# Kernel optimization log

Hardware: AMD Instinct MI355X
Metric: run time of the kernel (lower is better)

## Reference

```python
import jax, jax.numpy as jnp
import numpy as np

N_NODES = 50000
N_EDGES = 1600000
IN_CH = 128
HEADS = 4
OUT_PER_HEAD = 32  # out_channels // heads with concat=True
NEG_SLOPE = 0.2    # GATConv default leaky_relu slope
SOFTMAX_EPS = 1e-16  # PyG scatter-softmax denominator eps
LN_EPS = 1e-5


def setup_inputs() -> dict:
    key = jax.random.key(0)
    ks = jax.random.split(key, 8)
    x = jax.random.normal(ks[0], (N_NODES, IN_CH), dtype=jnp.float32)
    edge_index = jax.random.randint(ks[1], (2, N_EDGES), 0, N_NODES, dtype=jnp.int32)
    W = jax.random.normal(ks[2], (IN_CH, HEADS * OUT_PER_HEAD), dtype=jnp.float32) * (1.0 / np.sqrt(IN_CH))
    att_src = jax.random.normal(ks[3], (HEADS, OUT_PER_HEAD), dtype=jnp.float32) * 0.1
    att_dst = jax.random.normal(ks[4], (HEADS, OUT_PER_HEAD), dtype=jnp.float32) * 0.1
    bias = jnp.zeros((HEADS * OUT_PER_HEAD,), dtype=jnp.float32)
    gamma = jnp.ones((HEADS * OUT_PER_HEAD,), dtype=jnp.float32)
    beta = jnp.zeros((HEADS * OUT_PER_HEAD,), dtype=jnp.float32)
    return {"x": x, "edge_index": edge_index, "W": W, "att_src": att_src,
            "att_dst": att_dst, "bias": bias, "gamma": gamma, "beta": beta}


def reference(x, edge_index, W, att_src, att_dst, bias, gamma, beta):
    N = x.shape[0]
    H, C = att_src.shape
    # GATConv default add_self_loops=True
    loop = jnp.arange(N, dtype=edge_index.dtype)
    src = jnp.concatenate([edge_index[0], loop])  # message source j
    dst = jnp.concatenate([edge_index[1], loop])  # aggregation target i

    h = (x @ W).reshape(N, H, C)                      # [N,H,C]
    a_s = jnp.einsum('nhc,hc->nh', h, att_src)        # [N,H]
    a_d = jnp.einsum('nhc,hc->nh', h, att_dst)        # [N,H]

    logits = jax.nn.leaky_relu(a_s[src] + a_d[dst], NEG_SLOPE)  # [E,H]
    # segment softmax over edges grouped by destination node
    m = jax.ops.segment_max(logits, dst, num_segments=N)        # [N,H]
    m = jnp.where(jnp.isfinite(m), m, 0.0)
    e = jnp.exp(logits - m[dst])
    s = jax.ops.segment_sum(e, dst, num_segments=N)             # [N,H]
    alpha = e / (s[dst] + SOFTMAX_EPS)                          # [E,H]

    msg = h[src] * alpha[:, :, None]                            # [E,H,C]
    out = jax.ops.segment_sum(msg, dst, num_segments=N)         # [N,H,C]
    out = out.reshape(N, H * C) + bias

    mu = out.mean(axis=-1, keepdims=True)
    var = ((out - mu) ** 2).mean(axis=-1, keepdims=True)
    y = (out - mu) / jnp.sqrt(var + LN_EPS) * gamma + beta
    return jax.nn.elu(y)
```

## Files before the change

kernel.cpp:

```cpp
#include <hip/hip_runtime.h>
#include <hip/hip_bf16.h>

typedef __hip_bfloat16 bf16;
typedef unsigned int u32;
typedef unsigned short u16;
typedef __attribute__((ext_vector_type(8))) short bf16x8;
typedef __attribute__((ext_vector_type(4))) float f32x4;

constexpr int N   = 50000;
constexpr int E   = 1600000;
constexpr int C   = 128;
constexpr int H   = 4;
constexpr int NB  = 782;
constexpr int CAP = 2560;
constexpr int CHUNK = 6250;
constexpr float NEG  = 0.2f;
constexpr float SEPS = 1e-16f;
constexpr float LEPS = 1e-5f;

__device__ __forceinline__ float lo16(u32 v) { return __uint_as_float(v << 16); }
__device__ __forceinline__ float hi16(u32 v) { return __uint_as_float(v & 0xFFFF0000u); }
__device__ __forceinline__ u16 bfbits(float f) {
    __hip_bfloat16 h = __float2bfloat16(f);
    return *reinterpret_cast<u16*>(&h);
}

__global__ __launch_bounds__(256) void k0_wprep(
    const float* __restrict__ W, u16* __restrict__ wt_hi, u16* __restrict__ wt_lo)
{
    const int i = blockIdx.x * 256 + threadIdx.x;
    const int c = i >> 7, k = i & 127;
    const float w = W[k * 128 + c];
    const __hip_bfloat16 h = __float2bfloat16(w);
    const float fh = __bfloat162float(h);
    wt_hi[i] = *(const u16*)&h;
    wt_lo[i] = bfbits(w - fh);
}

__global__ __launch_bounds__(256) void k1_mfma(
    const float* __restrict__ x,
    const u16* __restrict__ wt_hi, const u16* __restrict__ wt_lo,
    const float* __restrict__ att_s, const float* __restrict__ att_d,
    u16* __restrict__ hb, float* __restrict__ as_, float* __restrict__ ad_)
{
    constexpr int LDX = 136;
    __shared__ u16 xhi[64 * LDX];
    __shared__ u16 xlo[64 * LDX];
    const int t  = threadIdx.x;
    const int m0 = blockIdx.x * 64;

#pragma unroll
    for (int it = 0; it < 8; ++it) {
        const int idx = it * 1024 + t * 4;
        const int r = idx >> 7, c = idx & 127;
        const int gr = min(m0 + r, N - 1);
        const float4 v = *(const float4*)(x + (size_t)gr * 128 + c);
        ushort4 sh, sl;
        {
            __hip_bfloat16 h0 = __float2bfloat16(v.x);
            __hip_bfloat16 h1 = __float2bfloat16(v.y);
            __hip_bfloat16 h2 = __float2bfloat16(v.z);
            __hip_bfloat16 h3 = __float2bfloat16(v.w);
            sh.x = *(u16*)&h0; sh.y = *(u16*)&h1; sh.z = *(u16*)&h2; sh.w = *(u16*)&h3;
            sl.x = bfbits(v.x - __bfloat162float(h0));
            sl.y = bfbits(v.y - __bfloat162float(h1));
            sl.z = bfbits(v.z - __bfloat162float(h2));
            sl.w = bfbits(v.w - __bfloat162float(h3));
        }
        *(ushort4*)(xhi + r * LDX + c) = sh;
        *(ushort4*)(xlo + r * LDX + c) = sl;
    }
    __syncthreads();

    const int lane = t & 63;
    const int w    = t >> 6;
    const int arow = w * 16 + (lane & 15);
    const int akg  = lane >> 4;
    const int bcol = lane & 15;
    const int aq   = lane >> 4;

    bf16x8 Ah[4], Al[4];
#pragma unroll
    for (int ks = 0; ks < 4; ++ks) {
        Ah[ks] = *(const bf16x8*)(xhi + arow * LDX + ks * 32 + akg * 8);
        Al[ks] = *(const bf16x8*)(xlo + arow * LDX + ks * 32 + akg * 8);
    }

    f32x4 acc[8];
#pragma unroll
    for (int nt = 0; nt < 8; ++nt) acc[nt] = f32x4{0.f, 0.f, 0.f, 0.f};

#pragma unroll
    for (int nt = 0; nt < 8; ++nt) {
        const u16* bp = wt_hi + (nt * 16 + bcol) * 128 + akg * 8;
        const u16* bq = wt_lo + (nt * 16 + bcol) * 128 + akg * 8;
#pragma unroll
        for (int ks = 0; ks < 4; ++ks) {
            const bf16x8 Bh = *(const bf16x8*)(bp + ks * 32);
            const bf16x8 Bl = *(const bf16x8*)(bq + ks * 32);
            acc[nt] = __builtin_amdgcn_mfma_f32_16x16x32_bf16(Ah[ks], Bh, acc[nt], 0, 0, 0);
            acc[nt] = __builtin_amdgcn_mfma_f32_16x16x32_bf16(Al[ks], Bh, acc[nt], 0, 0, 0);
            acc[nt] = __builtin_amdgcn_mfma_f32_16x16x32_bf16(Ah[ks], Bl, acc[nt], 0, 0, 0);
        }
    }

#pragma unroll
    for (int nt = 0; nt < 8; ++nt) {
        const int ch = nt * 16 + bcol;
#pragma unroll
        for (int r = 0; r < 4; ++r) {
            const int node = m0 + w * 16 + aq * 4 + r;
            if (node < N) hb[(size_t)node * 128 + ch] = bfbits(acc[nt][r]);
        }
    }

    float ps[4][4], pd[4][4];
#pragma unroll
    for (int h = 0; h < 4; ++h) {
        const float a0 = att_s[32 * h + bcol],      a1 = att_s[32 * h + 16 + bcol];
        const float d0 = att_d[32 * h + bcol],      d1 = att_d[32 * h + 16 + bcol];
#pragma unroll
        for (int r = 0; r < 4; ++r) {
            ps[h][r] = acc[2 * h][r] * a0 + acc[2 * h + 1][r] * a1;
            pd[h][r] = acc[2 * h][r] * d0 + acc[2 * h + 1][r] * d1;
        }
    }
#pragma unroll
    for (int off = 1; off < 16; off <<= 1) {
#pragma unroll
        for (int h = 0; h < 4; ++h)
#pragma unroll
            for (int r = 0; r < 4; ++r) {
                ps[h][r] += __shfl_xor(ps[h][r], off, 64);
                pd[h][r] += __shfl_xor(pd[h][r], off, 64);
            }
    }
    if (bcol == 0) {
#pragma unroll
        for (int r = 0; r < 4; ++r) {
            const int node = m0 + w * 16 + aq * 4 + r;
            if (node < N) {
#pragma unroll
                for (int h = 0; h < 4; ++h) {
                    as_[node * H + h] = ps[h][r];
                    ad_[node * H + h] = pd[h][r];
                }
            }
        }
    }
}

__global__ __launch_bounds__(256) void kbin(
    const int* __restrict__ ei, u32* __restrict__ gcur, u32* __restrict__ pairs)
{
    __shared__ u32 lcnt[NB], lbase[NB], lfill[NB];
    const int t = threadIdx.x;
    const int base = blockIdx.x * CHUNK;
    const int nE = min(CHUNK, E - base);
    for (int i = t; i < NB; i += 256) lcnt[i] = 0;
    __syncthreads();
    for (int i = t; i < nE; i += 256)
        atomicAdd(&lcnt[((u32)ei[E + base + i]) >> 6], 1u);
    __syncthreads();
    for (int i = t; i < NB; i += 256) {
        u32 cb = lcnt[i];
        lbase[i] = cb ? atomicAdd(&gcur[i], cb) : 0u;
        lfill[i] = 0u;
    }
    __syncthreads();
    for (int i = t; i < nE; i += 256) {
        u32 src = (u32)ei[base + i];
        u32 dst = (u32)ei[E + base + i];
        u32 b = dst >> 6;
        u32 pos = atomicAdd(&lfill[b], 1u);
        pairs[(size_t)b * CAP + lbase[b] + pos] = src | ((dst & 63u) << 16);
    }
}

__global__ __launch_bounds__(64) void kscan(
    const u32* __restrict__ gcur, u32* __restrict__ bbase, int* __restrict__ row_ptr)
{
    const int t = threadIdx.x;
    u32 vals[13];
    u32 s = 0;
#pragma unroll
    for (int i = 0; i < 13; ++i) {
        int idx = t * 13 + i;
        u32 v = (idx < NB) ? gcur[idx] : 0u;
        vals[i] = s; s += v;
    }
    u32 incl = s;
#pragma unroll
    for (int off = 1; off < 64; off <<= 1) {
        u32 u = __shfl_up(incl, off, 64);
        if (t >= off) incl += u;
    }
    const u32 excl = incl - s;
#pragma unroll
    for (int i = 0; i < 13; ++i) {
        int idx = t * 13 + i;
        if (idx < NB) bbase[idx] = excl + vals[i];
    }
    if (t == 0) row_ptr[N] = E;
}

__global__ __launch_bounds__(256) void kfill2(
    const u32* __restrict__ pairs, const u32* __restrict__ gcur,
    const u32* __restrict__ bbase, int* __restrict__ row_ptr, u16* __restrict__ col)
{
    __shared__ u32 spr[CAP];
    __shared__ u16 scol[CAP];
    __shared__ int jcnt[64], joff[64], jcur[64];
    const int b = blockIdx.x, t = threadIdx.x;
    const int cntb = (int)gcur[b];
    const int base = (int)bbase[b];
    if (t < 64) jcnt[t] = 0;
    const u32* pr = pairs + (size_t)b * CAP;
    for (int i = t; i < cntb; i += 256) spr[i] = pr[i];
    __syncthreads();
    for (int i = t; i < cntb; i += 256) atomicAdd(&jcnt[spr[i] >> 16], 1);
    __syncthreads();
    if (t < 64) {
        int v = jcnt[t], incl = v;
#pragma unroll
        for (int off = 1; off < 64; off <<= 1) {
            int u = __shfl_up(incl, off, 64);
            if (t >= off) incl += u;
        }
        joff[t] = incl - v;
        const int n = b * 64 + t;
        if (n < N) row_ptr[n] = base + joff[t];
        jcur[t] = 0;
    }
    __syncthreads();
    for (int i = t; i < cntb; i += 256) {
        const u32 p = spr[i];
        const int j = p >> 16;
        const int pos = atomicAdd(&jcur[j], 1);
        scol[joff[j] + pos] = (u16)(p & 0xFFFFu);
    }
    __syncthreads();
    for (int i = t; i < cntb; i += 256) col[base + i] = scol[i];
}

__global__ __launch_bounds__(256) void kd_agg_ln(
    const int* __restrict__ row_ptr, const u16* __restrict__ col,
    const u32* __restrict__ hb, const float* __restrict__ as_,
    const float* __restrict__ ad_,
    const float* __restrict__ bias, const float* __restrict__ gamma,
    const float* __restrict__ beta, float* __restrict__ out)
{
    __shared__ float wlds[4][64];
    const int tid  = threadIdx.x;
    const int lane = tid & 63;
    const int wv   = __builtin_amdgcn_readfirstlane(tid >> 6);
    const int n    = __builtin_amdgcn_readfirstlane((int)blockIdx.x * 4 + (tid >> 6));
    if (n >= N) return;

    const int head  = lane >> 4;
    const int eoff  = lane & 15;
    const int wbase = head << 4;
    float* __restrict__ wrow = wlds[wv];

    const float adn = ad_[n * H + head];
    const float asn = as_[n * H + head];

    float ls = asn + adn;
    ls = fmaxf(ls, NEG * ls);
    const float wself = __expf(ls);
    float den = (eoff == 0) ? wself : 0.f;
    const u32 hvs = hb[n * 64 + lane];
    float num0 = wself * lo16(hvs);
    float num1 = wself * hi16(hvs);

    const int k0  = row_ptr[n];
    const int deg = row_ptr[n + 1] - k0;
    const int ntiles = (deg + 15) >> 4;

    const int cnt0 = deg < 16 ? deg : 16;
    const int cnt1 = (deg - 16) < 16 ? (deg - 16) : 16;
    int colv_cur = (eoff < cnt0) ? (int)col[k0 + eoff]      : 0;
    int colv_nxt = (eoff < cnt1) ? (int)col[k0 + 16 + eoff] : 0;
    float a_cur  = as_[colv_cur * H + head];
    int cntc = cnt0, cntn = cnt1;

    int k = k0;
    for (int t = 0; t < ntiles; ++t, k += 16) {
        const int rem2 = deg - 16 * (t + 2);
        const int cnt2 = rem2 < 16 ? rem2 : 16;
        const int cf_raw = (int)col[k + 32 + eoff];
        const int colv_f = (eoff < cnt2) ? cf_raw : 0;

        float le = a_cur + adn;
        le = fmaxf(le, NEG * le);
        const float w = (eoff < cntc) ? __expf(le) : 0.f;
        den += w;
        wrow[lane] = w;
        const int colc = colv_cur;

#define GL(i) const u32* rp##i = hb + ((size_t)(u32)__builtin_amdgcn_readlane(colc, i) << 6); \
              const u32 v##i = rp##i[lane];
        GL(0) GL(1) GL(2) GL(3) GL(4) GL(5) GL(6) GL(7)
        GL(8) GL(9) GL(10) GL(11) GL(12) GL(13) GL(14) GL(15)
#undef GL
        __builtin_amdgcn_sched_barrier(0);

        const float a_n = as_[colv_nxt * H + head];
        __builtin_amdgcn_sched_barrier(0);

        {
            const float4 wa = *(const float4*)(wrow + wbase + 0);
            num0 = fmaf(wa.x, lo16(v0), num0);  num1 = fmaf(wa.x, hi16(v0), num1);
            num0 = fmaf(wa.y, lo16(v1), num0);  num1 = fmaf(wa.y, hi16(v1), num1);
            num0 = fmaf(wa.z, lo16(v2), num0);  num1 = fmaf(wa.z, hi16(v2), num1);
            num0 = fmaf(wa.w, lo16(v3), num0);  num1 = fmaf(wa.w, hi16(v3), num1);
            const float4 wb = *(const float4*)(wrow + wbase + 4);
            num0 = fmaf(wb.x, lo16(v4), num0);  num1 = fmaf(wb.x, hi16(v4), num1);
            num0 = fmaf(wb.y, lo16(v5), num0);  num1 = fmaf(wb.y, hi16(v5), num1);
            num0 = fmaf(wb.z, lo16(v6), num0);  num1 = fmaf(wb.z, hi16(v6), num1);
            num0 = fmaf(wb.w, lo16(v7), num0);  num1 = fmaf(wb.w, hi16(v7), num1);
            const float4 wc = *(const float4*)(wrow + wbase + 8);
            num0 = fmaf(wc.x, lo16(v8), num0);  num1 = fmaf(wc.x, hi16(v8), num1);
            num0 = fmaf(wc.y, lo16(v9), num0);  num1 = fmaf(wc.y, hi16(v9), num1);
            num0 = fmaf(wc.z, lo16(v10), num0); num1 = fmaf(wc.z, hi16(v10), num1);
            num0 = fmaf(wc.w, lo16(v11), num0); num1 = fmaf(wc.w, hi16(v11), num1);
            const float4 wd = *(const float4*)(wrow + wbase + 12);
            num0 = fmaf(wd.x, lo16(v12), num0); num1 = fmaf(wd.x, hi16(v12), num1);
            num0 = fmaf(wd.y, lo16(v13), num0); num1 = fmaf(wd.y, hi16(v13), num1);
            num0 = fmaf(wd.z, lo16(v14), num0); num1 = fmaf(wd.z, hi16(v14), num1);
            num0 = fmaf(wd.w, lo16(v15), num0); num1 = fmaf(wd.w, hi16(v15), num1);
        }

        colv_cur = colv_nxt; colv_nxt = colv_f;
        a_cur = a_n;
        cntc = cntn; cntn = cnt2;
    }

#pragma unroll
    for (int off = 1; off < 16; off <<= 1) den += __shfl_xor(den, off, 64);

    const int c0 = lane * 2;
    const float inv_den = 1.f / (den + SEPS);
    const float2 bi = *(const float2*)(bias + c0);
    float v0 = num0 * inv_den + bi.x;
    float v1 = num1 * inv_den + bi.y;

    float sum = v0 + v1;
#pragma unroll
    for (int off = 32; off; off >>= 1) sum += __shfl_xor(sum, off, 64);
    const float mu = sum * (1.0f / C);
    const float d0 = v0 - mu, d1 = v1 - mu;
    float sq = d0 * d0 + d1 * d1;
#pragma unroll
    for (int off = 32; off; off >>= 1) sq += __shfl_xor(sq, off, 64);
    const float inv = rsqrtf(sq * (1.0f / C) + LEPS);
    const float2 ga = *(const float2*)(gamma + c0);
    const float2 be = *(const float2*)(beta  + c0);
    float y0 = d0 * inv * ga.x + be.x;
    float y1 = d1 * inv * ga.y + be.y;
    y0 = y0 > 0.f ? y0 : __expf(y0) - 1.f;
    y1 = y1 > 0.f ? y1 : __expf(y1) - 1.f;
    float2 o; o.x = y0; o.y = y1;
    *(float2*)(out + (size_t)n * C + c0) = o;
}

extern "C" void kernel_launch(void* const* d_in, const int* in_sizes, int n_in,
                              void* d_out, int out_size, void* d_ws, size_t ws_size,
                              hipStream_t stream)
{
    const float* x     = (const float*)d_in[0];
    const int*   ei    = (const int*)  d_in[1];
    const float* W     = (const float*)d_in[2];
    const float* att_s = (const float*)d_in[3];
    const float* att_d = (const float*)d_in[4];
    const float* bias  = (const float*)d_in[5];
    const float* gamma = (const float*)d_in[6];
    const float* beta  = (const float*)d_in[7];
    float* out = (float*)d_out;

    char* p = (char*)d_ws;
    bf16*  hb      = (bf16*)p;   p += (size_t)N * C * sizeof(bf16);
    float* as_     = (float*)p;  p += (size_t)N * H * sizeof(float);
    float* ad_     = (float*)p;  p += (size_t)N * H * sizeof(float);
    u32*   pairs   = (u32*)p;    p += (size_t)NB * CAP * sizeof(u32);
    u16*   col     = (u16*)p;    p += ((size_t)(E + 64) * sizeof(u16) + 15) & ~(size_t)15;
    int*   row_ptr = (int*)p;    p += ((size_t)(N + 1) * sizeof(int) + 15) & ~(size_t)15;
    u32*   gcur    = (u32*)p;    p += (size_t)NB * sizeof(u32);
    u32*   bbase   = (u32*)p;    p += (((size_t)NB * sizeof(u32)) + 15) & ~(size_t)15;
    u16*   wt_hi   = (u16*)p;    p += (size_t)128 * 128 * sizeof(u16);
    u16*   wt_lo   = (u16*)p;

    hipMemsetAsync(gcur, 0, NB * sizeof(u32), stream);
    k0_wprep<<<64, 256, 0, stream>>>(W, wt_hi, wt_lo);
    k1_mfma<<<(N + 63) / 64, 256, 0, stream>>>(x, wt_hi, wt_lo, att_s, att_d,
                                               (u16*)hb, as_, ad_);
    kbin<<<E / CHUNK, 256, 0, stream>>>(ei, gcur, pairs);
    kscan<<<1, 64, 0, stream>>>(gcur, bbase, row_ptr);
    kfill2<<<NB, 256, 0, stream>>>(pairs, gcur, bbase, row_ptr, col);
    kd_agg_ln<<<(N * 64) / 256, 256, 0, stream>>>(
        row_ptr, col, (const u32*)hb, as_, ad_, bias, gamma, beta, out);
}
```

Baseline: 223.7 us.

## Fuse weight prep into GEMM, merge edge counting, use deterministic two-pass binning

The separate weight-split kernel is removed, and W is converted to bf16 hi/lo inside the GEMM directly from the fp32 global array. The edge-count pass is folded into the GEMM launch as extra blocks, each writing a per-chunk histogram. A per-bucket scan over chunks then gives every chunk exact offsets, so binning writes compact pairs with no global atomics, no memset and no fixed-capacity slots. This cuts the launch count and global atomic contention, but it adds redundant scans in kbinB and kfill2 and uncached strided loads of W in every GEMM block.

```diff
diff --git a/kernel.cpp b/kernel.cpp
--- a/kernel.cpp
+++ b/kernel.cpp
@@ -13,7 +13,9 @@
 constexpr int H   = 4;
 constexpr int NB  = 782;
 constexpr int CAP = 2560;
-constexpr int CHUNK = 6250;
+constexpr int NCH = 256;
+constexpr int CHUNK = E / NCH;
+constexpr int GEMM_BLOCKS = 782;
 constexpr float NEG  = 0.2f;
 constexpr float SEPS = 1e-16f;
 constexpr float LEPS = 1e-5f;
@@ -25,36 +27,41 @@
     return *reinterpret_cast<u16*>(&h);
 }
 
-__global__ __launch_bounds__(256) void k0_wprep(
-    const float* __restrict__ W, u16* __restrict__ wt_hi, u16* __restrict__ wt_lo)
-{
-    const int i = blockIdx.x * 256 + threadIdx.x;
-    const int c = i >> 7, k = i & 127;
-    const float w = W[k * 128 + c];
-    const __hip_bfloat16 h = __float2bfloat16(w);
-    const float fh = __bfloat162float(h);
-    wt_hi[i] = *(const u16*)&h;
-    wt_lo[i] = bfbits(w - fh);
-}
-
-__global__ __launch_bounds__(256) void k1_mfma(
-    const float* __restrict__ x,
-    const u16* __restrict__ wt_hi, const u16* __restrict__ wt_lo,
+__global__ __launch_bounds__(256) void f1_gemm_count(
+    const float* __restrict__ x, const float* __restrict__ W,
     const float* __restrict__ att_s, const float* __restrict__ att_d,
-    u16* __restrict__ hb, float* __restrict__ as_, float* __restrict__ ad_)
+    const int* __restrict__ ei,
+    u16* __restrict__ hb, float* __restrict__ as_, float* __restrict__ ad_,
+    u32* __restrict__ gcnt)
 {
     constexpr int LDX = 136;
-    __shared__ u16 xhi[64 * LDX];
-    __shared__ u16 xlo[64 * LDX];
-    const int t  = threadIdx.x;
+    union Smem {
+        struct { u16 xhi[64 * LDX]; u16 xlo[64 * LDX]; } g;
+        u32 lcnt[NB];
+    };
+    __shared__ Smem sm;
+    const int t = threadIdx.x;
+
+    if (blockIdx.x >= GEMM_BLOCKS) {
+        const int c = blockIdx.x - GEMM_BLOCKS;
+        const int base = c * CHUNK;
+        for (int i = t; i < NB; i += 256) sm.lcnt[i] = 0;
+        __syncthreads();
+        for (int i = t; i < CHUNK; i += 256)
+            atomicAdd(&sm.lcnt[((u32)ei[E + base + i]) >> 6], 1u);
+        __syncthreads();
+        for (int i = t; i < NB; i += 256) gcnt[i * NCH + c] = sm.lcnt[i];
+        return;
+    }
+
     const int m0 = blockIdx.x * 64;
 
 #pragma unroll
     for (int it = 0; it < 8; ++it) {
         const int idx = it * 1024 + t * 4;
-        const int r = idx >> 7, c = idx & 127;
+        const int r = idx >> 7, cc = idx & 127;
         const int gr = min(m0 + r, N - 1);
-        const float4 v = *(const float4*)(x + (size_t)gr * 128 + c);
+        const float4 v = *(const float4*)(x + (size_t)gr * 128 + cc);
         ushort4 sh, sl;
         {
             __hip_bfloat16 h0 = __float2bfloat16(v.x);
@@ -67,8 +74,8 @@
             sl.z = bfbits(v.z - __bfloat162float(h2));
             sl.w = bfbits(v.w - __bfloat162float(h3));
         }
-        *(ushort4*)(xhi + r * LDX + c) = sh;
-        *(ushort4*)(xlo + r * LDX + c) = sl;
+        *(ushort4*)(sm.g.xhi + r * LDX + cc) = sh;
+        *(ushort4*)(sm.g.xlo + r * LDX + cc) = sl;
     }
     __syncthreads();
 
@@ -82,8 +89,8 @@
     bf16x8 Ah[4], Al[4];
 #pragma unroll
     for (int ks = 0; ks < 4; ++ks) {
-        Ah[ks] = *(const bf16x8*)(xhi + arow * LDX + ks * 32 + akg * 8);
-        Al[ks] = *(const bf16x8*)(xlo + arow * LDX + ks * 32 + akg * 8);
+        Ah[ks] = *(const bf16x8*)(sm.g.xhi + arow * LDX + ks * 32 + akg * 8);
+        Al[ks] = *(const bf16x8*)(sm.g.xlo + arow * LDX + ks * 32 + akg * 8);
     }
 
     f32x4 acc[8];
@@ -92,12 +99,19 @@
 
 #pragma unroll
     for (int nt = 0; nt < 8; ++nt) {
-        const u16* bp = wt_hi + (nt * 16 + bcol) * 128 + akg * 8;
-        const u16* bq = wt_lo + (nt * 16 + bcol) * 128 + akg * 8;
+        const int ch = nt * 16 + bcol;
 #pragma unroll
         for (int ks = 0; ks < 4; ++ks) {
-            const bf16x8 Bh = *(const bf16x8*)(bp + ks * 32);
-            const bf16x8 Bl = *(const bf16x8*)(bq + ks * 32);
+            const int kk = ks * 32 + akg * 8;
+            bf16x8 Bh, Bl;
+#pragma unroll
+            for (int j = 0; j < 8; ++j) {
+                const float wv = W[(size_t)(kk + j) * 128 + ch];
+                const __hip_bfloat16 hh = __float2bfloat16(wv);
+                Bh[j] = *(const short*)&hh;
+                const __hip_bfloat16 hl = __float2bfloat16(wv - __bfloat162float(hh));
+                Bl[j] = *(const short*)&hl;
+            }
             acc[nt] = __builtin_amdgcn_mfma_f32_16x16x32_bf16(Ah[ks], Bh, acc[nt], 0, 0, 0);
             acc[nt] = __builtin_amdgcn_mfma_f32_16x16x32_bf16(Al[ks], Bh, acc[nt], 0, 0, 0);
             acc[nt] = __builtin_amdgcn_mfma_f32_16x16x32_bf16(Ah[ks], Bl, acc[nt], 0, 0, 0);
@@ -117,8 +131,8 @@
     float ps[4][4], pd[4][4];
 #pragma unroll
     for (int h = 0; h < 4; ++h) {
-        const float a0 = att_s[32 * h + bcol],      a1 = att_s[32 * h + 16 + bcol];
-        const float d0 = att_d[32 * h + bcol],      d1 = att_d[32 * h + 16 + bcol];
+        const float a0 = att_s[32 * h + bcol], a1 = att_s[32 * h + 16 + bcol];
+        const float d0 = att_d[32 * h + bcol], d1 = att_d[32 * h + 16 + bcol];
 #pragma unroll
         for (int r = 0; r < 4; ++r) {
             ps[h][r] = acc[2 * h][r] * a0 + acc[2 * h + 1][r] * a1;
@@ -150,72 +164,91 @@
     }
 }
 
-__global__ __launch_bounds__(256) void kbin(
-    const int* __restrict__ ei, u32* __restrict__ gcur, u32* __restrict__ pairs)
-{
-    __shared__ u32 lcnt[NB], lbase[NB], lfill[NB];
-    const int t = threadIdx.x;
-    const int base = blockIdx.x * CHUNK;
-    const int nE = min(CHUNK, E - base);
-    for (int i = t; i < NB; i += 256) lcnt[i] = 0;
-    __syncthreads();
-    for (int i = t; i < nE; i += 256)
-        atomicAdd(&lcnt[((u32)ei[E + base + i]) >> 6], 1u);
-    __syncthreads();
-    for (int i = t; i < NB; i += 256) {
-        u32 cb = lcnt[i];
-        lbase[i] = cb ? atomicAdd(&gcur[i], cb) : 0u;
-        lfill[i] = 0u;
-    }
-    __syncthreads();
-    for (int i = t; i < nE; i += 256) {
-        u32 src = (u32)ei[base + i];
-        u32 dst = (u32)ei[E + base + i];
-        u32 b = dst >> 6;
-        u32 pos = atomicAdd(&lfill[b], 1u);
-        pairs[(size_t)b * CAP + lbase[b] + pos] = src | ((dst & 63u) << 16);
-    }
-}
-
-__global__ __launch_bounds__(64) void kscan(
-    const u32* __restrict__ gcur, u32* __restrict__ bbase, int* __restrict__ row_ptr)
-{
-    const int t = threadIdx.x;
-    u32 vals[13];
-    u32 s = 0;
-#pragma unroll
-    for (int i = 0; i < 13; ++i) {
-        int idx = t * 13 + i;
-        u32 v = (idx < NB) ? gcur[idx] : 0u;
-        vals[i] = s; s += v;
-    }
-    u32 incl = s;
+__global__ __launch_bounds__(256) void s2a_scan(
+    const u32* __restrict__ gcnt, u32* __restrict__ gbase, u32* __restrict__ tot)
+{
+    __shared__ u32 wsum[4];
+    const int b = blockIdx.x, t = threadIdx.x, lane = t & 63, w = t >> 6;
+    const u32 v = gcnt[b * NCH + t];
+    u32 incl = v;
 #pragma unroll
     for (int off = 1; off < 64; off <<= 1) {
         u32 u = __shfl_up(incl, off, 64);
-        if (t >= off) incl += u;
-    }
-    const u32 excl = incl - s;
-#pragma unroll
-    for (int i = 0; i < 13; ++i) {
-        int idx = t * 13 + i;
-        if (idx < NB) bbase[idx] = excl + vals[i];
-    }
-    if (t == 0) row_ptr[N] = E;
+        if (lane >= off) incl += u;
+    }
+    if (lane == 63) wsum[w] = incl;
+    __syncthreads();
+    u32 wpre = 0;
+#pragma unroll
+    for (int i = 0; i < 4; ++i) if (i < w) wpre += wsum[i];
+    gbase[b * NCH + t] = wpre + incl - v;
+    if (t == 255) tot[b] = wpre + incl;
+}
+
+__global__ __launch_bounds__(256) void kbinB(
+    const int* __restrict__ ei, const u32* __restrict__ gbase,
+    const u32* __restrict__ tot, u32* __restrict__ pairs)
+{
+    __shared__ u32 sl[NB];
+    __shared__ u32 lfill[NB];
+    __shared__ u32 wsum[4];
+    const int t = threadIdx.x, lane = t & 63, w = t >> 6;
+    const int c = blockIdx.x;
+
+    u32 carry = 0;
+    for (int q = 0; q < 4; ++q) {
+        const int idx = q * 256 + t;
+        const u32 v = (idx < NB) ? tot[idx] : 0u;
+        u32 incl = v;
+#pragma unroll
+        for (int off = 1; off < 64; off <<= 1) {
+            u32 u = __shfl_up(incl, off, 64);
+            if (lane >= off) incl += u;
+        }
+        if (lane == 63) wsum[w] = incl;
+        __syncthreads();
+        u32 wpre = 0, wtot = 0;
+#pragma unroll
+        for (int i = 0; i < 4; ++i) { const u32 s = wsum[i]; wtot += s; if (i < w) wpre += s; }
+        if (idx < NB) sl[idx] = carry + wpre + (incl - v) + gbase[(size_t)idx * NCH + c];
+        carry += wtot;
+        __syncthreads();
+    }
+    for (int i = t; i < NB; i += 256) lfill[i] = 0u;
+    __syncthreads();
+
+    const int base = c * CHUNK;
+    for (int i = t; i < CHUNK; i += 256) {
+        const u32 src = (u32)ei[base + i];
+        const u32 dst = (u32)ei[E + base + i];
+        const u32 b = dst >> 6;
+        const u32 pos = atomicAdd(&lfill[b], 1u);
+        pairs[sl[b] + pos] = src | ((dst & 63u) << 16);
+    }
 }
 
 __global__ __launch_bounds__(256) void kfill2(
-    const u32* __restrict__ pairs, const u32* __restrict__ gcur,
-    const u32* __restrict__ bbase, int* __restrict__ row_ptr, u16* __restrict__ col)
+    const u32* __restrict__ pairs, const u32* __restrict__ tot,
+    int* __restrict__ row_ptr, u16* __restrict__ col)
 {
     __shared__ u32 spr[CAP];
     __shared__ u16 scol[CAP];
     __shared__ int jcnt[64], joff[64], jcur[64];
+    __shared__ u32 rsum[4];
     const int b = blockIdx.x, t = threadIdx.x;
-    const int cntb = (int)gcur[b];
-    const int base = (int)bbase[b];
+    const int lane = t & 63, w = t >> 6;
+
+    u32 part = 0;
+    for (int i = t; i < b; i += 256) part += tot[i];
+#pragma unroll
+    for (int off = 32; off; off >>= 1) part += __shfl_xor(part, off, 64);
+    if (lane == 0) rsum[w] = part;
     if (t < 64) jcnt[t] = 0;
-    const u32* pr = pairs + (size_t)b * CAP;
+    __syncthreads();
+    const int base = (int)(rsum[0] + rsum[1] + rsum[2] + rsum[3]);
+    const int cntb = (int)tot[b];
+
+    const u32* pr = pairs + base;
     for (int i = t; i < cntb; i += 256) spr[i] = pr[i];
     __syncthreads();
     for (int i = t; i < cntb; i += 256) atomicAdd(&jcnt[spr[i] >> 16], 1);
@@ -241,6 +274,7 @@
     }
     __syncthreads();
     for (int i = t; i < cntb; i += 256) col[base + i] = scol[i];
+    if (b == 0 && t == 0) row_ptr[N] = E;
 }
 
 __global__ __launch_bounds__(256) void kd_agg_ln(
@@ -382,21 +416,18 @@
     bf16*  hb      = (bf16*)p;   p += (size_t)N * C * sizeof(bf16);
     float* as_     = (float*)p;  p += (size_t)N * H * sizeof(float);
     float* ad_     = (float*)p;  p += (size_t)N * H * sizeof(float);
-    u32*   pairs   = (u32*)p;    p += (size_t)NB * CAP * sizeof(u32);
+    u32*   pairs   = (u32*)p;    p += (size_t)E * sizeof(u32);
     u16*   col     = (u16*)p;    p += ((size_t)(E + 64) * sizeof(u16) + 15) & ~(size_t)15;
     int*   row_ptr = (int*)p;    p += ((size_t)(N + 1) * sizeof(int) + 15) & ~(size_t)15;
-    u32*   gcur    = (u32*)p;    p += (size_t)NB * sizeof(u32);
-    u32*   bbase   = (u32*)p;    p += (((size_t)NB * sizeof(u32)) + 15) & ~(size_t)15;
-    u16*   wt_hi   = (u16*)p;    p += (size_t)128 * 128 * sizeof(u16);
-    u16*   wt_lo   = (u16*)p;
-
-    hipMemsetAsync(gcur, 0, NB * sizeof(u32), stream);
-    k0_wprep<<<64, 256, 0, stream>>>(W, wt_hi, wt_lo);
-    k1_mfma<<<(N + 63) / 64, 256, 0, stream>>>(x, wt_hi, wt_lo, att_s, att_d,
-                                               (u16*)hb, as_, ad_);
-    kbin<<<E / CHUNK, 256, 0, stream>>>(ei, gcur, pairs);
-    kscan<<<1, 64, 0, stream>>>(gcur, bbase, row_ptr);
-    kfill2<<<NB, 256, 0, stream>>>(pairs, gcur, bbase, row_ptr, col);
+    u32*   gcnt    = (u32*)p;    p += (size_t)NB * NCH * sizeof(u32);
+    u32*   gbase   = (u32*)p;    p += (size_t)NB * NCH * sizeof(u32);
+    u32*   tot     = (u32*)p;
+
+    f1_gemm_count<<<GEMM_BLOCKS + NCH, 256, 0, stream>>>(
+        x, W, att_s, att_d, ei, (u16*)hb, as_, ad_, gcnt);
+    s2a_scan<<<NB, 256, 0, stream>>>(gcnt, gbase, tot);
+    kbinB<<<NCH, 256, 0, stream>>>(ei, gbase, tot, pairs);
+    kfill2<<<NB, 256, 0, stream>>>(pairs, tot, row_ptr, col);
     kd_agg_ln<<<(N * 64) / 256, 256, 0, stream>>>(
         row_ptr, col, (const u32*)hb, as_, ad_, bias, gamma, beta, out);
 }
```

After: 214.6 us. 1.04x faster.
